# Performance work log

Hardware: AMD Instinct MI355X
Metric: run time of the kernel (lower is better)

## Reference

```python
import jax, jax.numpy as jnp
import numpy as np

EMBED_DIM = 512
LQ, LA, T, B = 32, 16, 32, 8192
BN_EPS = 1e-5


def _masked_mean(x, lens):
    # x: [L, B, D] seq-first; lens: [B] int. Mean over the first lens[b] steps.
    L = x.shape[0]
    mask = (jnp.arange(L)[:, None] < lens[None, :]).astype(x.dtype)  # [L, B]
    s = jnp.einsum('lb,lbd->bd', mask, x)
    return s / lens.astype(x.dtype)[:, None]


def setup_inputs() -> dict:
    key = jax.random.key(0)
    ks = jax.random.split(key, 12)
    D = EMBED_DIM
    inp = {
        'question_embedding_v': jax.random.normal(ks[0], (LQ, B, D), jnp.float32),
        'visual_embedding_qu': jax.random.normal(ks[1], (T, B, D), jnp.float32),
        'question_len': jax.random.randint(ks[2], (B,), 1, LQ + 1),
        'answer_embedding_v_expand': jax.random.normal(ks[3], (LA, B, D), jnp.float32),
        'visual_embedding_an_expand': jax.random.normal(ks[4], (T, B, D), jnp.float32),
        'answers_len': jax.random.randint(ks[5], (B,), 1, LA + 1),
    }
    # Classifier params (xavier-normal linears, zero bias; BN gamma=1, beta=0)
    def xavier(k, fan_out, fan_in):
        std = (2.0 / (fan_in + fan_out)) ** 0.5
        return std * jax.random.normal(k, (fan_out, fan_in), jnp.float32)
    inp['W1'] = xavier(ks[6], D, 4 * D)
    inp['b1'] = jnp.zeros((D,), jnp.float32)
    inp['gamma'] = jnp.ones((D,), jnp.float32)
    inp['beta'] = jnp.zeros((D,), jnp.float32)
    inp['W2'] = xavier(ks[7], 1, D)
    inp['b2'] = jnp.zeros((1,), jnp.float32)
    return inp


def reference(question_embedding_v, visual_embedding_qu, question_len,
              answer_embedding_v_expand, visual_embedding_an_expand, answers_len,
              W1, b1, gamma, beta, W2, b2):
    q = _masked_mean(question_embedding_v, question_len)            # [B, D]
    vq = jnp.mean(visual_embedding_qu, axis=0)                      # [B, D]
    a = _masked_mean(answer_embedding_v_expand, answers_len)        # [B, D]
    va = jnp.mean(visual_embedding_an_expand, axis=0)               # [B, D]
    out = jnp.concatenate([q, vq, a, va], axis=1)                   # [B, 4D]
    # Dropout treated as identity (eval / deterministic baseline).
    h = out @ W1.T + b1                                             # [B, D]
    h = jax.nn.gelu(h, approximate=False)                           # torch nn.GELU (exact erf)
    # BatchNorm1d in training mode: biased batch statistics over B.
    mu = jnp.mean(h, axis=0)
    var = jnp.mean(jnp.square(h - mu), axis=0)
    h = (h - mu) * jax.lax.rsqrt(var + BN_EPS) * gamma + beta
    logits = h @ W2.T + b2                                          # [B, 1]
    return logits
```

## Files before the change

kernel.cpp:

```cpp
#include <hip/hip_runtime.h>
#include <hip/hip_bf16.h>
#include <math.h>

typedef unsigned short u16;
typedef unsigned int   u32;
typedef short  short8 __attribute__((ext_vector_type(8)));
typedef float  f32x4  __attribute__((ext_vector_type(4)));

#define EMB 512
#define BB  8192
#define KDIM 2048

__device__ inline u16 f2b(float f) {
    union { float f; u32 u; } v; v.f = f;
    u32 r = v.u + 0x7fffu + ((v.u >> 16) & 1u);
    return (u16)(r >> 16);
}

__device__ inline f32x4 ntload(const float* p) {
    return __builtin_nontemporal_load((const f32x4*)p);
}

__global__ __launch_bounds__(256) void k_w1(const float4* __restrict__ w, u16* __restrict__ o) {
    int i = blockIdx.x * 256 + threadIdx.x;
    float4 v = w[i];
    u32 lo = (u32)f2b(v.x) | ((u32)f2b(v.y) << 16);
    u32 hi = (u32)f2b(v.z) | ((u32)f2b(v.w) << 16);
    *(uint2*)(o + (size_t)i * 4) = make_uint2(lo, hi);
}

__global__ __launch_bounds__(256) void k_meanfull(const float* __restrict__ vqu,
                                                  const float* __restrict__ van,
                                                  u16* __restrict__ pooled)
{
    const int tid = threadIdx.x;
    const int ln  = tid & 63;
    int bid = blockIdx.x;
    const float* src; int sec;
    if (bid < 256) { src = vqu; sec = 1; }
    else           { src = van; sec = 3; bid -= 256; }
    const int g = bid * 4 + (tid >> 6);
    const size_t rowf = (size_t)BB * EMB;

    f32x4 acc[16];
    #pragma unroll
    for (int j = 0; j < 16; ++j) acc[j] = (f32x4){0.f, 0.f, 0.f, 0.f};

    const float* p0 = src + (size_t)g * 4096 + ln * 4;
    for (int l = 0; l < 32; ++l) {
        const float* p = p0 + (size_t)l * rowf;
        f32x4 v[16];
        #pragma unroll
        for (int j = 0; j < 16; ++j) v[j] = ntload(p + j * 256);
        #pragma unroll
        for (int j = 0; j < 16; ++j) acc[j] += v[j];
    }

    const int bA = g * 8;
    const float iv = 1.0f / 32.0f;
    #pragma unroll
    for (int j = 0; j < 16; ++j) {
        f32x4 a = acc[j];
        u16* dst = pooled + (size_t)(bA + (j >> 1)) * KDIM + sec * EMB
                 + (j & 1) * 256 + ln * 4;
        *(uint2*)dst = make_uint2((u32)f2b(a.x*iv) | ((u32)f2b(a.y*iv) << 16),
                                  (u32)f2b(a.z*iv) | ((u32)f2b(a.w*iv) << 16));
    }
}

__global__ __launch_bounds__(256) void k_meanmask(
    const float* __restrict__ qv, const int* __restrict__ qlen,
    const float* __restrict__ av, const int* __restrict__ alen,
    u16* __restrict__ pooled)
{
    const int tid  = threadIdx.x;
    const int w    = tid >> 6;
    const int lane = tid & 63;
    const int bA   = blockIdx.x * 16 + w * 4;
    const size_t rowf = (size_t)BB * EMB;

    {
        const int n0 = __builtin_amdgcn_readfirstlane(qlen[bA]);
        const int n1 = __builtin_amdgcn_readfirstlane(qlen[bA + 1]);
        const int n2 = __builtin_amdgcn_readfirstlane(qlen[bA + 2]);
        const int n3 = __builtin_amdgcn_readfirstlane(qlen[bA + 3]);
        int mx = n0 > n1 ? n0 : n1;
        mx = mx > n2 ? mx : n2; mx = mx > n3 ? mx : n3;
        f32x4 a0 = {0,0,0,0}, b0 = a0, a1 = a0, b1 = a0,
              a2 = a0, b2 = a0, a3 = a0, b3 = a0;
        const float* p = qv + (size_t)bA * EMB + lane * 4;
        for (int l = 0; l < mx; ++l) {
            const float* r = p + (size_t)l * rowf;
            if (l < n0) { f32x4 v = ntload(r),        u = ntload(r + 256);  a0 += v; b0 += u; }
            if (l < n1) { f32x4 v = ntload(r + 512),  u = ntload(r + 768);  a1 += v; b1 += u; }
            if (l < n2) { f32x4 v = ntload(r + 1024), u = ntload(r + 1280); a2 += v; b2 += u; }
            if (l < n3) { f32x4 v = ntload(r + 1536), u = ntload(r + 1792); a3 += v; b3 += u; }
        }
        const float i0 = 1.0f/(float)n0, i1 = 1.0f/(float)n1,
                    i2 = 1.0f/(float)n2, i3 = 1.0f/(float)n3;
        u16* d0 = pooled + (size_t)(bA    ) * KDIM + lane * 4;
        u16* d1 = pooled + (size_t)(bA + 1) * KDIM + lane * 4;
        u16* d2 = pooled + (size_t)(bA + 2) * KDIM + lane * 4;
        u16* d3 = pooled + (size_t)(bA + 3) * KDIM + lane * 4;
        *(uint2*)(d0      ) = make_uint2((u32)f2b(a0.x*i0) | ((u32)f2b(a0.y*i0) << 16),
                                         (u32)f2b(a0.z*i0) | ((u32)f2b(a0.w*i0) << 16));
        *(uint2*)(d0 + 256) = make_uint2((u32)f2b(b0.x*i0) | ((u32)f2b(b0.y*i0) << 16),
                                         (u32)f2b(b0.z*i0) | ((u32)f2b(b0.w*i0) << 16));
        *(uint2*)(d1      ) = make_uint2((u32)f2b(a1.x*i1) | ((u32)f2b(a1.y*i1) << 16),
                                         (u32)f2b(a1.z*i1) | ((u32)f2b(a1.w*i1) << 16));
        *(uint2*)(d1 + 256) = make_uint2((u32)f2b(b1.x*i1) | ((u32)f2b(b1.y*i1) << 16),
                                         (u32)f2b(b1.z*i1) | ((u32)f2b(b1.w*i1) << 16));
        *(uint2*)(d2      ) = make_uint2((u32)f2b(a2.x*i2) | ((u32)f2b(a2.y*i2) << 16),
                                         (u32)f2b(a2.z*i2) | ((u32)f2b(a2.w*i2) << 16));
        *(uint2*)(d2 + 256) = make_uint2((u32)f2b(b2.x*i2) | ((u32)f2b(b2.y*i2) << 16),
                                         (u32)f2b(b2.z*i2) | ((u32)f2b(b2.w*i2) << 16));
        *(uint2*)(d3      ) = make_uint2((u32)f2b(a3.x*i3) | ((u32)f2b(a3.y*i3) << 16),
                                         (u32)f2b(a3.z*i3) | ((u32)f2b(a3.w*i3) << 16));
        *(uint2*)(d3 + 256) = make_uint2((u32)f2b(b3.x*i3) | ((u32)f2b(b3.y*i3) << 16),
                                         (u32)f2b(b3.z*i3) | ((u32)f2b(b3.w*i3) << 16));
    }
    {
        const int n0 = __builtin_amdgcn_readfirstlane(alen[bA]);
        const int n1 = __builtin_amdgcn_readfirstlane(alen[bA + 1]);
        const int n2 = __builtin_amdgcn_readfirstlane(alen[bA + 2]);
        const int n3 = __builtin_amdgcn_readfirstlane(alen[bA + 3]);
        int mx = n0 > n1 ? n0 : n1;
        mx = mx > n2 ? mx : n2; mx = mx > n3 ? mx : n3;
        f32x4 a0 = {0,0,0,0}, b0 = a0, a1 = a0, b1 = a0,
              a2 = a0, b2 = a0, a3 = a0, b3 = a0;
        const float* p = av + (size_t)bA * EMB + lane * 4;
        for (int l = 0; l < mx; ++l) {
            const float* r = p + (size_t)l * rowf;
            if (l < n0) { f32x4 v = ntload(r),        u = ntload(r + 256);  a0 += v; b0 += u; }
            if (l < n1) { f32x4 v = ntload(r + 512),  u = ntload(r + 768);  a1 += v; b1 += u; }
            if (l < n2) { f32x4 v = ntload(r + 1024), u = ntload(r + 1280); a2 += v; b2 += u; }
            if (l < n3) { f32x4 v = ntload(r + 1536), u = ntload(r + 1792); a3 += v; b3 += u; }
        }
        const float i0 = 1.0f/(float)n0, i1 = 1.0f/(float)n1,
                    i2 = 1.0f/(float)n2, i3 = 1.0f/(float)n3;
        u16* d0 = pooled + (size_t)(bA    ) * KDIM + 2 * EMB + lane * 4;
        u16* d1 = pooled + (size_t)(bA + 1) * KDIM + 2 * EMB + lane * 4;
        u16* d2 = pooled + (size_t)(bA + 2) * KDIM + 2 * EMB + lane * 4;
        u16* d3 = pooled + (size_t)(bA + 3) * KDIM + 2 * EMB + lane * 4;
        *(uint2*)(d0      ) = make_uint2((u32)f2b(a0.x*i0) | ((u32)f2b(a0.y*i0) << 16),
                                         (u32)f2b(a0.z*i0) | ((u32)f2b(a0.w*i0) << 16));
        *(uint2*)(d0 + 256) = make_uint2((u32)f2b(b0.x*i0) | ((u32)f2b(b0.y*i0) << 16),
                                         (u32)f2b(b0.z*i0) | ((u32)f2b(b0.w*i0) << 16));
        *(uint2*)(d1      ) = make_uint2((u32)f2b(a1.x*i1) | ((u32)f2b(a1.y*i1) << 16),
                                         (u32)f2b(a1.z*i1) | ((u32)f2b(a1.w*i1) << 16));
        *(uint2*)(d1 + 256) = make_uint2((u32)f2b(b1.x*i1) | ((u32)f2b(b1.y*i1) << 16),
                                         (u32)f2b(b1.z*i1) | ((u32)f2b(b1.w*i1) << 16));
        *(uint2*)(d2      ) = make_uint2((u32)f2b(a2.x*i2) | ((u32)f2b(a2.y*i2) << 16),
                                         (u32)f2b(a2.z*i2) | ((u32)f2b(a2.w*i2) << 16));
        *(uint2*)(d2 + 256) = make_uint2((u32)f2b(b2.x*i2) | ((u32)f2b(b2.y*i2) << 16),
                                         (u32)f2b(b2.z*i2) | ((u32)f2b(b2.w*i2) << 16));
        *(uint2*)(d3      ) = make_uint2((u32)f2b(a3.x*i3) | ((u32)f2b(a3.y*i3) << 16),
                                         (u32)f2b(a3.z*i3) | ((u32)f2b(a3.w*i3) << 16));
        *(uint2*)(d3 + 256) = make_uint2((u32)f2b(b3.x*i3) | ((u32)f2b(b3.y*i3) << 16),
                                         (u32)f2b(b3.z*i3) | ((u32)f2b(b3.w*i3) << 16));
    }
}

#define GBM 64
#define GBN 128
#define GBK 64
__global__ __launch_bounds__(256) void k_gemm(
    const u16* __restrict__ A, const u16* __restrict__ Bw,
    const float* __restrict__ bias, float* __restrict__ H)
{
    __shared__ u16 As[GBM * GBK];
    __shared__ u16 Bs[GBN * GBK];

    const int tid  = threadIdx.x;
    const int lane = tid & 63;
    const int wid  = tid >> 6;
    const int brow = blockIdx.y * GBM;
    const int bcol = blockIdx.x * GBN;

    const int lrow = lane & 15;
    const int lko  = (lane >> 4) * 8;

    f32x4 acc[4][2];
    #pragma unroll
    for (int m = 0; m < 4; ++m)
        #pragma unroll
        for (int n = 0; n < 2; ++n)
            acc[m][n] = (f32x4){0.f, 0.f, 0.f, 0.f};

    for (int kt = 0; kt < KDIM / GBK; ++kt) {
        const int k0 = kt * GBK;
        #pragma unroll
        for (int i = 0; i < 2; ++i) {
            int flat = i * 256 + tid;
            int row  = flat >> 3;
            int c8   = (flat & 7) * 8;
            const u16* src = A + (size_t)(brow + row) * KDIM + k0 + c8;
            u16* dst = &As[flat * 8];
            __builtin_amdgcn_global_load_lds(
                (const __attribute__((address_space(1))) void*)src,
                (__attribute__((address_space(3))) void*)dst, 16, 0, 0);
        }
        #pragma unroll
        for (int i = 0; i < 4; ++i) {
            int flat = i * 256 + tid;
            int row  = flat >> 3;
            int c8   = (flat & 7) * 8;
            const u16* src = Bw + (size_t)(bcol + row) * KDIM + k0 + c8;
            u16* dst = &Bs[flat * 8];
            __builtin_amdgcn_global_load_lds(
                (const __attribute__((address_space(1))) void*)src,
                (__attribute__((address_space(3))) void*)dst, 16, 0, 0);
        }
        __syncthreads();
        #pragma unroll
        for (int kk = 0; kk < 2; ++kk) {
            short8 bfrag[2];
            #pragma unroll
            for (int n = 0; n < 2; ++n)
                bfrag[n] = *(const short8*)&Bs[(wid * 32 + n * 16 + lrow) * GBK + kk * 32 + lko];
            #pragma unroll
            for (int m = 0; m < 4; ++m) {
                short8 afrag = *(const short8*)&As[(m * 16 + lrow) * GBK + kk * 32 + lko];
                #pragma unroll
                for (int n = 0; n < 2; ++n)
                    acc[m][n] = __builtin_amdgcn_mfma_f32_16x16x32_bf16(
                        afrag, bfrag[n], acc[m][n], 0, 0, 0);
            }
        }
        __syncthreads();
    }

    #pragma unroll
    for (int m = 0; m < 4; ++m) {
        const int row0 = brow + m * 16 + (lane >> 4) * 4;
        #pragma unroll
        for (int n = 0; n < 2; ++n) {
            const int col = bcol + wid * 32 + n * 16 + (lane & 15);
            const float bv = bias[col];
            #pragma unroll
            for (int r = 0; r < 4; ++r) {
                float x = acc[m][n][r] + bv;
                float g = 0.5f * x * (1.0f + erff(x * 0.70710678118654752f));
                H[(size_t)(row0 + r) * EMB + col] = g;
            }
        }
    }
}

__global__ __launch_bounds__(512) void k_stats(const float* __restrict__ H,
                                               float* __restrict__ psum,
                                               float* __restrict__ psq)
{
    const int f = threadIdx.x;
    const int j = blockIdx.x;
    const float* p = H + (size_t)j * 32 * EMB + f;
    float s = 0.f, ss = 0.f;
    #pragma unroll 4
    for (int r = 0; r < 32; ++r) {
        float v = p[(size_t)r * EMB];
        s += v; ss += v * v;
    }
    psum[j * EMB + f] = s;
    psq [j * EMB + f] = ss;
}

__global__ __launch_bounds__(512) void k_fin(const float* __restrict__ psum,
                                             const float* __restrict__ psq,
                                             const float* __restrict__ gamma,
                                             const float* __restrict__ beta,
                                             const float* __restrict__ W2,
                                             const float* __restrict__ b2,
                                             float* __restrict__ coeff)
{
    const int f = threadIdx.x;
    float s = 0.f, ss = 0.f;
    for (int j = 0; j < 256; ++j) { s += psum[j * EMB + f]; ss += psq[j * EMB + f]; }
    const float invB = 1.0f / 8192.0f;
    float mu  = s * invB;
    float var = ss * invB - mu * mu;
    float rs  = rsqrtf(var + 1e-5f);
    float c   = gamma[f] * rs * W2[f];
    coeff[f]  = c;
    float kterm = beta[f] * W2[f] - mu * c;

    __shared__ float red[512];
    red[f] = kterm;
    __syncthreads();
    for (int s2 = 256; s2 > 0; s2 >>= 1) {
        if (f < s2) red[f] += red[f + s2];
        __syncthreads();
    }
    if (f == 0) coeff[512] = red[0] + b2[0];
}

__global__ __launch_bounds__(64) void k_logits(const float* __restrict__ H,
                                               const float* __restrict__ coeff,
                                               float* __restrict__ out)
{
    const int b = blockIdx.x;
    const int l = threadIdx.x;
    const float4* hp = (const float4*)(H + (size_t)b * EMB);
    const float4* cp = (const float4*)coeff;
    float4 h0 = hp[l],      c0 = cp[l];
    float4 h1 = hp[l + 64], c1 = cp[l + 64];
    float p = h0.x * c0.x + h0.y * c0.y + h0.z * c0.z + h0.w * c0.w
            + h1.x * c1.x + h1.y * c1.y + h1.z * c1.z + h1.w * c1.w;
    #pragma unroll
    for (int off = 32; off > 0; off >>= 1) p += __shfl_down(p, off);
    if (l == 0) out[b] = p + coeff[512];
}

extern "C" void kernel_launch(void* const* d_in, const int* in_sizes, int n_in,
                              void* d_out, int out_size, void* d_ws, size_t ws_size,
                              hipStream_t stream) {
    (void)in_sizes; (void)n_in; (void)out_size; (void)ws_size;
    const float* qv    = (const float*)d_in[0];
    const float* vqu   = (const float*)d_in[1];
    const int*   qlen  = (const int*)d_in[2];
    const float* av    = (const float*)d_in[3];
    const float* van   = (const float*)d_in[4];
    const int*   alen  = (const int*)d_in[5];
    const float* W1    = (const float*)d_in[6];
    const float* b1    = (const float*)d_in[7];
    const float* gamma = (const float*)d_in[8];
    const float* beta  = (const float*)d_in[9];
    const float* W2    = (const float*)d_in[10];
    const float* b2    = (const float*)d_in[11];
    float* out = (float*)d_out;

    char* ws = (char*)d_ws;
    u16*   pooled = (u16*)(ws);
    u16*   w1b    = (u16*)(ws + 33554432);
    float* H      = (float*)(ws + 35651584);
    float* psum   = (float*)(ws + 52428800);
    float* psq    = (float*)(ws + 52953088);
    float* coeff  = (float*)(ws + 53477376);

    k_w1      <<<dim3(1024),   dim3(256), 0, stream>>>((const float4*)W1, w1b);
    k_meanfull<<<dim3(512),    dim3(256), 0, stream>>>(vqu, van, pooled);
    k_meanmask<<<dim3(512),    dim3(256), 0, stream>>>(qv, qlen, av, alen, pooled);
    k_gemm    <<<dim3(4, 128), dim3(256), 0, stream>>>(pooled, w1b, b1, H);
    k_stats   <<<dim3(256),    dim3(512), 0, stream>>>(H, psum, psq);
    k_fin     <<<dim3(1),      dim3(512), 0, stream>>>(psum, psq, gamma, beta, W2, b2, coeff);
    k_logits  <<<dim3(8192),   dim3(64),  0, stream>>>(H, coeff, out);
}
```

Measured before the change: 345.7 us.

## Enlarge GEMM tile to 128x128 with 2x2 wave layout and XOR-swizzled LDS

Doubles the GEMM block tile in M so each wave computes a 64x64 sub-tile, raising MFMA work per LDS fragment load. The LDS layout is XOR-swizzled per row on both the async global-to-LDS writes and the fragment reads to reduce bank conflicts. The grid halves to 256 blocks, which lowers parallelism and may leave CUs with only one block each. Accumulator registers grow accordingly.

```diff
diff --git a/kernel.cpp b/kernel.cpp
--- a/kernel.cpp
+++ b/kernel.cpp
@@ -161,7 +161,7 @@
     }
 }
 
-#define GBM 64
+#define GBM 128
 #define GBN 128
 #define GBK 64
 __global__ __launch_bounds__(256) void k_gemm(
@@ -174,55 +174,54 @@
     const int tid  = threadIdx.x;
     const int lane = tid & 63;
     const int wid  = tid >> 6;
+    const int wr   = wid >> 1;
+    const int wc   = wid & 1;
     const int brow = blockIdx.y * GBM;
     const int bcol = blockIdx.x * GBN;
 
     const int lrow = lane & 15;
     const int lko  = (lane >> 4) * 8;
-
-    f32x4 acc[4][2];
+    const int gsub = lko >> 3;
+
+    f32x4 acc[4][4];
     #pragma unroll
     for (int m = 0; m < 4; ++m)
         #pragma unroll
-        for (int n = 0; n < 2; ++n)
+        for (int n = 0; n < 4; ++n)
             acc[m][n] = (f32x4){0.f, 0.f, 0.f, 0.f};
 
     for (int kt = 0; kt < KDIM / GBK; ++kt) {
         const int k0 = kt * GBK;
         #pragma unroll
-        for (int i = 0; i < 2; ++i) {
-            int flat = i * 256 + tid;
-            int row  = flat >> 3;
-            int c8   = (flat & 7) * 8;
-            const u16* src = A + (size_t)(brow + row) * KDIM + k0 + c8;
-            u16* dst = &As[flat * 8];
+        for (int i = 0; i < 4; ++i) {
+            int f   = i * 256 + tid;
+            int row = f >> 3;
+            int gl  = (f & 7) ^ (row & 7);
+            const u16* srcA = A  + (size_t)(brow + row) * KDIM + k0 + gl * 8;
+            const u16* srcB = Bw + (size_t)(bcol + row) * KDIM + k0 + gl * 8;
             __builtin_amdgcn_global_load_lds(
-                (const __attribute__((address_space(1))) void*)src,
-                (__attribute__((address_space(3))) void*)dst, 16, 0, 0);
-        }
-        #pragma unroll
-        for (int i = 0; i < 4; ++i) {
-            int flat = i * 256 + tid;
-            int row  = flat >> 3;
-            int c8   = (flat & 7) * 8;
-            const u16* src = Bw + (size_t)(bcol + row) * KDIM + k0 + c8;
-            u16* dst = &Bs[flat * 8];
+                (const __attribute__((address_space(1))) void*)srcA,
+                (__attribute__((address_space(3))) void*)&As[f * 8], 16, 0, 0);
             __builtin_amdgcn_global_load_lds(
-                (const __attribute__((address_space(1))) void*)src,
-                (__attribute__((address_space(3))) void*)dst, 16, 0, 0);
+                (const __attribute__((address_space(1))) void*)srcB,
+                (__attribute__((address_space(3))) void*)&Bs[f * 8], 16, 0, 0);
         }
         __syncthreads();
         #pragma unroll
         for (int kk = 0; kk < 2; ++kk) {
-            short8 bfrag[2];
+            const int glog = kk * 4 + gsub;
+            short8 bfrag[4];
             #pragma unroll
-            for (int n = 0; n < 2; ++n)
-                bfrag[n] = *(const short8*)&Bs[(wid * 32 + n * 16 + lrow) * GBK + kk * 32 + lko];
+            for (int n = 0; n < 4; ++n) {
+                int row = wc * 64 + n * 16 + lrow;
+                bfrag[n] = *(const short8*)&Bs[row * GBK + ((glog ^ (row & 7)) * 8)];
+            }
             #pragma unroll
             for (int m = 0; m < 4; ++m) {
-                short8 afrag = *(const short8*)&As[(m * 16 + lrow) * GBK + kk * 32 + lko];
+                int row = wr * 64 + m * 16 + lrow;
+                short8 afrag = *(const short8*)&As[row * GBK + ((glog ^ (row & 7)) * 8)];
                 #pragma unroll
-                for (int n = 0; n < 2; ++n)
+                for (int n = 0; n < 4; ++n)
                     acc[m][n] = __builtin_amdgcn_mfma_f32_16x16x32_bf16(
                         afrag, bfrag[n], acc[m][n], 0, 0, 0);
             }
@@ -232,10 +231,10 @@
 
     #pragma unroll
     for (int m = 0; m < 4; ++m) {
-        const int row0 = brow + m * 16 + (lane >> 4) * 4;
-        #pragma unroll
-        for (int n = 0; n < 2; ++n) {
-            const int col = bcol + wid * 32 + n * 16 + (lane & 15);
+        const int row0 = brow + wr * 64 + m * 16 + (lane >> 4) * 4;
+        #pragma unroll
+        for (int n = 0; n < 4; ++n) {
+            const int col = bcol + wc * 64 + n * 16 + (lane & 15);
             const float bv = bias[col];
             #pragma unroll
             for (int r = 0; r < 4; ++r) {
@@ -339,7 +338,7 @@
     k_w1      <<<dim3(1024),   dim3(256), 0, stream>>>((const float4*)W1, w1b);
     k_meanfull<<<dim3(512),    dim3(256), 0, stream>>>(vqu, van, pooled);
     k_meanmask<<<dim3(512),    dim3(256), 0, stream>>>(qv, qlen, av, alen, pooled);
-    k_gemm    <<<dim3(4, 128), dim3(256), 0, stream>>>(pooled, w1b, b1, H);
+    k_gemm    <<<dim3(4, 64),  dim3(256), 0, stream>>>(pooled, w1b, b1, H);
     k_stats   <<<dim3(256),    dim3(512), 0, stream>>>(H, psum, psq);
     k_fin     <<<dim3(1),      dim3(512), 0, stream>>>(psum, psq, gamma, beta, W2, b2, coeff);
     k_logits  <<<dim3(8192),   dim3(64),  0, stream>>>(H, coeff, out);
```

After: 345.9 us. About the same (+0.1%).
